# Kernel tuning notes

Hardware: AMD Instinct MI355X
Metric: run time of the kernel (lower is better)

The kernel has to match this reference:

```python
import jax, jax.numpy as jnp
import numpy as np

DIM = 128
HEADS = 4
DIM_HEAD = 32
HIDDEN = HEADS * DIM_HEAD  # 128
EPS = 1e-5


def setup_inputs() -> dict:
    key = jax.random.key(0)
    k0, k1, k2, k3 = jax.random.split(key, 4)
    b, h, w = 8, 128, 128
    x = jax.random.normal(k0, (b, DIM, h, w), dtype=jnp.float32)
    # 1x1 conv weights stored as [out_ch, in_ch]
    w_qkv = jax.random.normal(k1, (HIDDEN * 3, DIM), dtype=jnp.float32) * (1.0 / np.sqrt(DIM))
    w_out = jax.random.normal(k2, (DIM, HIDDEN), dtype=jnp.float32) * (1.0 / np.sqrt(HIDDEN))
    b_out = jnp.zeros((DIM,), dtype=jnp.float32)
    alpha = jnp.ones((DIM,), dtype=jnp.float32)
    beta = jnp.zeros((DIM,), dtype=jnp.float32)
    return {"x": x, "w_qkv": w_qkv, "w_out": w_out, "b_out": b_out,
            "alpha": alpha, "beta": beta}


def reference(x, w_qkv, w_out, b_out, alpha, beta):
    b, c, h, w = x.shape
    n = h * w
    scale = DIM_HEAD ** (-0.5)
    # 1x1 conv QKV (bias=False) == channel GEMM
    qkv = jnp.einsum('bchw,oc->bohw', x, w_qkv)  # [b, 3*HIDDEN, h, w]
    q, k, v = jnp.split(qkv, 3, axis=1)
    rs = lambda t: t.reshape(b, HEADS, DIM_HEAD, n)  # [b, heads, d, N]
    q = jax.nn.softmax(rs(q), axis=-2) * scale  # softmax over dim_head axis
    k = jax.nn.softmax(rs(k), axis=-1)          # softmax over spatial axis
    v = rs(v) / n
    # context[dk, dv] = sum_n k[dk, n] * v[dv, n]   (tiny d x d matrix)
    context = jnp.einsum('bhkn,bhvn->bhkv', k, v)
    # out[dv, n] = sum_dk context[dk, dv] * q[dk, n]
    out = jnp.einsum('bhkv,bhkn->bhvn', context, q)
    out = out.reshape(b, HIDDEN, h, w)
    # to_out: 1x1 conv with bias, then channel LayerNorm
    out = jnp.einsum('bchw,oc->bohw', out, w_out) + b_out[None, :, None, None]
    mean = jnp.mean(out, axis=1, keepdims=True)
    var = jnp.var(out, axis=1, keepdims=True)  # unbiased=False
    out = (out - mean) / jnp.sqrt(var + EPS)
    return out * alpha[None, :, None, None] + beta[None, :, None, None]
```

## Files before the change

### kernel.cpp

```cpp
#include <hip/hip_runtime.h>
#include <math.h>

#define B_ 8
#define C_ 128
#define N_ 16384
#define SCALE_ 0.17677669529663687f
#define EPS_ 1e-5f

#define KV_STRIDE 36
#define XU_STRIDE 68
#define REC_ 4224

typedef _Float16 half8 __attribute__((ext_vector_type(8)));
typedef float floatx4 __attribute__((ext_vector_type(4)));

static __device__ inline unsigned short f16bits(float v) {
  _Float16 h = (_Float16)v;
  return __builtin_bit_cast(unsigned short, h);
}

static __device__ inline void pack2(float a0, float a1,
                                    unsigned int& hp, unsigned int& lp) {
  _Float16 h0 = (_Float16)a0;
  _Float16 h1 = (_Float16)a1;
  float l0f = (a0 - (float)h0) * 2048.0f;
  float l1f = (a1 - (float)h1) * 2048.0f;
  hp = ((unsigned int)__builtin_bit_cast(unsigned short, h1) << 16) |
       (unsigned int)__builtin_bit_cast(unsigned short, h0);
  lp = ((unsigned int)f16bits(l1f) << 16) | (unsigned int)f16bits(l0f);
}

static __device__ inline void split8(const float* p, half8& hi, half8& lo) {
  float4 f0 = *(const float4*)p;
  float4 f1 = *(const float4*)(p + 4);
  float fv[8] = {f0.x, f0.y, f0.z, f0.w, f1.x, f1.y, f1.z, f1.w};
#pragma unroll
  for (int j = 0; j < 8; ++j) {
    _Float16 hj = (_Float16)fv[j];
    hi[j] = hj;
    lo[j] = (_Float16)((fv[j] - (float)hj) * 2048.0f);
  }
}

__global__ __launch_bounds__(1024, 4) void lin_attn_ctx(
    const float* __restrict__ x, const float* __restrict__ wqkv,
    float* __restrict__ Ws)
{
  __shared__ __align__(16) unsigned int xhiu[32 * XU_STRIDE];
  __shared__ __align__(16) unsigned int xlou[32 * XU_STRIDE];
  __shared__ __align__(16) float ks[128 * KV_STRIDE];
  __shared__ __align__(16) float vs[128 * KV_STRIDE];

  const int t = threadIdx.x;
  const int bpb = gridDim.x / B_;
  const int b = blockIdx.x / bpb;
  const int blk = blockIdx.x - b * bpb;
  const int nchunks = 512 / bpb;
  const int pbase = blk * (nchunks << 5);

  const int lane = t & 63;
  const int wave = t >> 6;
  const int l15 = lane & 15;
  const int quad = lane >> 4;

  half8 ahi[4], alo[4];
#pragma unroll
  for (int s = 0; s < 4; ++s)
    split8(wqkv + (size_t)(128 + (wave << 4) + l15) * C_ + (s << 5) + (quad << 3),
           ahi[s], alo[s]);

  const int hj = wave >> 2;
  const int at = (wave >> 1) & 1;
  const int bt = wave & 1;
  floatx4 pacc1 = (floatx4){0.f, 0.f, 0.f, 0.f};
  floatx4 pacc2 = (floatx4){0.f, 0.f, 0.f, 0.f};
  float sacc[4] = {0.f, 0.f, 0.f, 0.f};

  const float* xb = x + ((size_t)b * C_) * N_;
  const int kp0 = t >> 4;
  const int pq0 = (t & 15) << 1;

  float2 fa0, fa1;
  {
    const float* p = xb + pbase + pq0;
    fa0 = *(const float2*)(p + (size_t)(2 * kp0) * N_);
    fa1 = *(const float2*)(p + (size_t)(2 * kp0 + 1) * N_);
  }

  for (int c4 = 0; c4 < nchunks; ++c4) {
    __syncthreads();

    half8 eh, el, vh, vl;
    if (c4 > 0) {
      split8(&ks[((hj << 5) + (at << 4) + l15) * KV_STRIDE + (quad << 3)], eh, el);
      split8(&vs[((hj << 5) + (bt << 4) + l15) * KV_STRIDE + (quad << 3)], vh, vl);
    }

    {
      float a0[2] = {fa0.x, fa0.y};
      float a1[2] = {fa1.x, fa1.y};
#pragma unroll
      for (int j = 0; j < 2; ++j) {
        unsigned int hp, lp;
        pack2(a0[j], a1[j], hp, lp);
        xhiu[(pq0 + j) * XU_STRIDE + kp0] = hp;
        xlou[(pq0 + j) * XU_STRIDE + kp0] = lp;
      }
    }

    if (c4 > 0) {
      pacc1 = __builtin_amdgcn_mfma_f32_16x16x32_f16(eh, vh, pacc1, 0, 0, 0);
      pacc2 = __builtin_amdgcn_mfma_f32_16x16x32_f16(eh, vl, pacc2, 0, 0, 0);
      pacc2 = __builtin_amdgcn_mfma_f32_16x16x32_f16(el, vh, pacc2, 0, 0, 0);
    }

    __syncthreads();

    if (c4 + 1 < nchunks) {
      const float* p = xb + pbase + ((c4 + 1) << 5) + pq0;
      fa0 = *(const float2*)(p + (size_t)(2 * kp0) * N_);
      fa1 = *(const float2*)(p + (size_t)(2 * kp0 + 1) * N_);
    }

    floatx4 acc1[2], acc2[2];
#pragma unroll
    for (int c = 0; c < 2; ++c) {
      acc1[c] = (floatx4){0.f, 0.f, 0.f, 0.f};
      acc2[c] = (floatx4){0.f, 0.f, 0.f, 0.f};
    }
    __builtin_amdgcn_s_setprio(1);
#pragma unroll
    for (int s = 0; s < 4; ++s) {
#pragma unroll
      for (int c = 0; c < 2; ++c) {
        int off = ((c << 4) + l15) * XU_STRIDE + (s << 4) + (quad << 2);
        half8 bh = __builtin_bit_cast(half8, *(const uint4*)&xhiu[off]);
        half8 bl = __builtin_bit_cast(half8, *(const uint4*)&xlou[off]);
        acc1[c] = __builtin_amdgcn_mfma_f32_16x16x32_f16(ahi[s], bh, acc1[c], 0, 0, 0);
        acc2[c] = __builtin_amdgcn_mfma_f32_16x16x32_f16(ahi[s], bl, acc2[c], 0, 0, 0);
        acc2[c] = __builtin_amdgcn_mfma_f32_16x16x32_f16(alo[s], bh, acc2[c], 0, 0, 0);
      }
    }
    __builtin_amdgcn_s_setprio(0);

    if (wave < 8) {
#pragma unroll
      for (int c = 0; c < 2; ++c) {
        int px = (c << 4) + l15;
#pragma unroll
        for (int reg = 0; reg < 4; ++reg) {
          float val = acc1[c][reg] + acc2[c][reg] * (1.0f / 2048.0f);
          int row = (wave << 4) + (quad << 2) + reg;
          float e = __expf(val);
          ks[row * KV_STRIDE + px] = e;
          sacc[reg] += e;
        }
      }
    } else {
#pragma unroll
      for (int c = 0; c < 2; ++c) {
        int px = (c << 4) + l15;
#pragma unroll
        for (int reg = 0; reg < 4; ++reg) {
          float val = acc1[c][reg] + acc2[c][reg] * (1.0f / 2048.0f);
          int row = ((wave - 8) << 4) + (quad << 2) + reg;
          vs[row * KV_STRIDE + px] = val;
        }
      }
    }
  }

  __syncthreads();
  {
    half8 eh, el, vh, vl;
    split8(&ks[((hj << 5) + (at << 4) + l15) * KV_STRIDE + (quad << 3)], eh, el);
    split8(&vs[((hj << 5) + (bt << 4) + l15) * KV_STRIDE + (quad << 3)], vh, vl);
    pacc1 = __builtin_amdgcn_mfma_f32_16x16x32_f16(eh, vh, pacc1, 0, 0, 0);
    pacc2 = __builtin_amdgcn_mfma_f32_16x16x32_f16(eh, vl, pacc2, 0, 0, 0);
    pacc2 = __builtin_amdgcn_mfma_f32_16x16x32_f16(el, vh, pacc2, 0, 0, 0);
  }

  {
    float* rec = Ws + (size_t)blockIdx.x * REC_;
#pragma unroll
    for (int reg = 0; reg < 4; ++reg) {
      int dk = (at << 4) + (quad << 2) + reg;
      int dv = (bt << 4) + l15;
      rec[(((hj << 5) + dk) << 5) + dv] =
          pacc1[reg] + pacc2[reg] * (1.0f / 2048.0f);
    }
    if (wave < 8) {
#pragma unroll
      for (int reg = 0; reg < 4; ++reg) {
        float s = sacc[reg];
        s += __shfl_xor(s, 1);
        s += __shfl_xor(s, 2);
        s += __shfl_xor(s, 4);
        s += __shfl_xor(s, 8);
        sacc[reg] = s;
      }
      if (l15 == 0) {
#pragma unroll
        for (int reg = 0; reg < 4; ++reg)
          rec[4096 + (wave << 4) + (quad << 2) + reg] = sacc[reg];
      }
    }
  }
}

__global__ void lin_attn_redg(const float* __restrict__ Ws, int slots,
                              const float* __restrict__ wout,
                              float* __restrict__ G)
{
  __shared__ float p2[256];
  __shared__ float cx[128];
  __shared__ float ss[4];

  const int t = threadIdx.x;
  const int b = blockIdx.x >> 5;
  const int seg = blockIdx.x & 31;
  const int R0 = seg << 2;
  const int hs = slots >> 1;

  {
    const int e = t & 127;
    const int half = t >> 7;
    const float* src = Ws + ((size_t)b * slots + (size_t)half * hs) * REC_ +
                       R0 * 32 + e;
    float s = 0.f;
    for (int k = 0; k < hs; ++k) s += src[(size_t)k * REC_];
    p2[half * 128 + e] = s;
  }
  {
    const int row4 = t >> 6;
    const int lane = t & 63;
    float sv = (lane < slots)
             ? Ws[((size_t)b * slots + lane) * REC_ + 4096 + R0 + row4] : 0.f;
    sv += __shfl_xor(sv, 1);
    sv += __shfl_xor(sv, 2);
    sv += __shfl_xor(sv, 4);
    sv += __shfl_xor(sv, 8);
    sv += __shfl_xor(sv, 16);
    sv += __shfl_xor(sv, 32);
    if (lane == 0) ss[row4] = sv;
  }
  __syncthreads();
  if (t < 128) {
    cx[t] = (p2[t] + p2[128 + t]) / (ss[t >> 5] * 16384.f);
  }
  __syncthreads();
  {
    const int o = t >> 1;
    const int pr = t & 1;
#pragma unroll
    for (int p = 0; p < 2; ++p) {
      const int row4 = pr * 2 + p;
      const int grow = R0 + row4;
      const int h = grow >> 5;
      const float* wrow = wout + (size_t)o * 128 + h * 32;
      const float* crow = &cx[row4 * 32];
      float s = 0.f;
#pragma unroll
      for (int q = 0; q < 8; ++q) {
        float4 w4 = *(const float4*)&wrow[q * 4];
        float4 c4 = *(const float4*)&crow[q * 4];
        s += w4.x * c4.x + w4.y * c4.y + w4.z * c4.z + w4.w * c4.w;
      }
      G[(size_t)b * 16384 + (size_t)o * 128 + grow] = s * SCALE_;
    }
  }
}

__global__ __launch_bounds__(256, 2) void lin_attn_out(
    const float* __restrict__ x, const float* __restrict__ wqkv,
    const float* __restrict__ G, const float* __restrict__ bout,
    const float* __restrict__ alpha, const float* __restrict__ beta,
    float* __restrict__ out)
{
  __shared__ __align__(16) unsigned int xh[2][32 * XU_STRIDE];
  __shared__ __align__(16) unsigned int xl[2][32 * XU_STRIDE];
  __shared__ __align__(16) unsigned int qhiu[32 * XU_STRIDE];
  __shared__ __align__(16) unsigned int qlou[32 * XU_STRIDE];
  __shared__ float red_s[128];
  __shared__ float red_q[128];

  const int t = threadIdx.x;
  const int bpb = gridDim.x / B_;
  const int b = blockIdx.x / bpb;
  const int blk = blockIdx.x - b * bpb;
  const int nchunks = 512 / bpb;
  const int pbase = blk * (nchunks << 5);

  const int lane = t & 63;
  const int wave = t >> 6;
  const int l15 = lane & 15;
  const int quad = lane >> 4;

  half8 qhiA[2][4], qloA[2][4], ghiA[2][4], gloA[2][4];
#pragma unroll
  for (int r = 0; r < 2; ++r) {
#pragma unroll
    for (int s = 0; s < 4; ++s) {
      const int m = (wave << 5) + (r << 4) + l15;
      split8(wqkv + (size_t)m * C_ + (s << 5) + (quad << 3), qhiA[r][s], qloA[r][s]);
      split8(G + (size_t)b * 16384 + (size_t)m * 128 + (s << 5) + (quad << 3),
             ghiA[r][s], gloA[r][s]);
    }
  }

  float bch[8], ach[8], bech[8];
#pragma unroll
  for (int r = 0; r < 2; ++r)
#pragma unroll
    for (int reg = 0; reg < 4; ++reg) {
      int ch = (wave << 5) + (r << 4) + (quad << 2) + reg;
      bch[r * 4 + reg] = bout[ch];
      ach[r * 4 + reg] = alpha[ch];
      bech[r * 4 + reg] = beta[ch];
    }

  const float* xb = x + ((size_t)b * C_) * N_;
  const int kp0 = t >> 3;
  const int pq0 = (t & 7) << 2;
  float4 fa0, fa1, fb0, fb1;

  {
    const float* p = xb + pbase + pq0;
    fa0 = *(const float4*)(p + (size_t)(2 * kp0) * N_);
    fa1 = *(const float4*)(p + (size_t)(2 * kp0 + 1) * N_);
    fb0 = *(const float4*)(p + (size_t)(2 * kp0 + 64) * N_);
    fb1 = *(const float4*)(p + (size_t)(2 * kp0 + 65) * N_);
    float a0[4] = {fa0.x, fa0.y, fa0.z, fa0.w};
    float a1[4] = {fa1.x, fa1.y, fa1.z, fa1.w};
    float c0[4] = {fb0.x, fb0.y, fb0.z, fb0.w};
    float c1[4] = {fb1.x, fb1.y, fb1.z, fb1.w};
#pragma unroll
    for (int j = 0; j < 4; ++j) {
      unsigned int hp, lp;
      pack2(a0[j], a1[j], hp, lp);
      xh[0][(pq0 + j) * XU_STRIDE + kp0] = hp;
      xl[0][(pq0 + j) * XU_STRIDE + kp0] = lp;
      pack2(c0[j], c1[j], hp, lp);
      xh[0][(pq0 + j) * XU_STRIDE + kp0 + 32] = hp;
      xl[0][(pq0 + j) * XU_STRIDE + kp0 + 32] = lp;
    }
  }
  __syncthreads();

  float yv[2][8];

  for (int c4 = 0; c4 < nchunks; ++c4) {
    const int cur = c4 & 1;
    const int nxt = cur ^ 1;

    if (c4 + 1 < nchunks) {
      const float* p = xb + pbase + ((c4 + 1) << 5) + pq0;
      fa0 = *(const float4*)(p + (size_t)(2 * kp0) * N_);
      fa1 = *(const float4*)(p + (size_t)(2 * kp0 + 1) * N_);
      fb0 = *(const float4*)(p + (size_t)(2 * kp0 + 64) * N_);
      fb1 = *(const float4*)(p + (size_t)(2 * kp0 + 65) * N_);
    }

    floatx4 a1a[2][2], a2a[2][2];
#pragma unroll
    for (int r = 0; r < 2; ++r)
#pragma unroll
      for (int c = 0; c < 2; ++c) {
        a1a[r][c] = (floatx4){0.f, 0.f, 0.f, 0.f};
        a2a[r][c] = (floatx4){0.f, 0.f, 0.f, 0.f};
      }
    __builtin_amdgcn_s_setprio(1);
#pragma unroll
    for (int s = 0; s < 4; ++s) {
#pragma unroll
      for (int c = 0; c < 2; ++c) {
        int off = ((c << 4) + l15) * XU_STRIDE + (s << 4) + (quad << 2);
        half8 bh = __builtin_bit_cast(half8, *(const uint4*)&xh[cur][off]);
        half8 bl = __builtin_bit_cast(half8, *(const uint4*)&xl[cur][off]);
#pragma unroll
        for (int r = 0; r < 2; ++r) {
          a1a[r][c] = __builtin_amdgcn_mfma_f32_16x16x32_f16(qhiA[r][s], bh, a1a[r][c], 0, 0, 0);
          a2a[r][c] = __builtin_amdgcn_mfma_f32_16x16x32_f16(qhiA[r][s], bl, a2a[r][c], 0, 0, 0);
          a2a[r][c] = __builtin_amdgcn_mfma_f32_16x16x32_f16(qloA[r][s], bh, a2a[r][c], 0, 0, 0);
        }
      }
    }
    __builtin_amdgcn_s_setprio(0);

    float eq[2][8];
#pragma unroll
    for (int c = 0; c < 2; ++c) {
      float qv[8];
#pragma unroll
      for (int r = 0; r < 2; ++r)
#pragma unroll
        for (int reg = 0; reg < 4; ++reg)
          qv[r * 4 + reg] = a1a[r][c][reg] + a2a[r][c][reg] * (1.0f / 2048.0f);
      float mx = fmaxf(fmaxf(fmaxf(qv[0], qv[1]), fmaxf(qv[2], qv[3])),
                       fmaxf(fmaxf(qv[4], qv[5]), fmaxf(qv[6], qv[7])));
      mx = fmaxf(mx, __shfl_xor(mx, 16));
      mx = fmaxf(mx, __shfl_xor(mx, 32));
      float ss = 0.f;
#pragma unroll
      for (int j = 0; j < 8; ++j) { eq[c][j] = __expf(qv[j] - mx); ss += eq[c][j]; }
      ss += __shfl_xor(ss, 16);
      ss += __shfl_xor(ss, 32);
      float inv = 1.0f / ss;
#pragma unroll
      for (int j = 0; j < 8; ++j) eq[c][j] *= inv;
    }
    __syncthreads();

    if (c4 > 0) {
      float* ob = out + ((size_t)b * C_) * N_ + pbase + ((c4 - 1) << 5);
#pragma unroll
      for (int c = 0; c < 2; ++c) {
        int px = (c << 4) + l15;
        float ts = red_s[px] + red_s[32 + px] + red_s[64 + px] + red_s[96 + px];
        float tq = red_q[px] + red_q[32 + px] + red_q[64 + px] + red_q[96 + px];
        float mean = ts * (1.f / 128.f);
        float var = tq * (1.f / 128.f) - mean * mean;
        float rstd = 1.f / sqrtf(var + EPS_);
#pragma unroll
        for (int r = 0; r < 2; ++r)
#pragma unroll
          for (int reg = 0; reg < 4; ++reg) {
            int ch = (wave << 5) + (r << 4) + (quad << 2) + reg;
            ob[(size_t)ch * N_ + px] =
                (yv[c][r * 4 + reg] - mean) * rstd * ach[r * 4 + reg] + bech[r * 4 + reg];
          }
      }
    }

#pragma unroll
    for (int c = 0; c < 2; ++c) {
      int px = (c << 4) + l15;
#pragma unroll
      for (int r = 0; r < 2; ++r) {
        unsigned int h0, l0, h1, l1;
        pack2(eq[c][r * 4 + 0], eq[c][r * 4 + 1], h0, l0);
        pack2(eq[c][r * 4 + 2], eq[c][r * 4 + 3], h1, l1);
        int kp = (wave << 4) + (r << 3) + (quad << 1);
        uint2 hu; hu.x = h0; hu.y = h1;
        uint2 lu; lu.x = l0; lu.y = l1;
        *(uint2*)&qhiu[px * XU_STRIDE + kp] = hu;
        *(uint2*)&qlou[px * XU_STRIDE + kp] = lu;
      }
    }
    if (c4 + 1 < nchunks) {
      float a0[4] = {fa0.x, fa0.y, fa0.z, fa0.w};
      float a1[4] = {fa1.x, fa1.y, fa1.z, fa1.w};
      float c0[4] = {fb0.x, fb0.y, fb0.z, fb0.w};
      float c1[4] = {fb1.x, fb1.y, fb1.z, fb1.w};
#pragma unroll
      for (int j = 0; j < 4; ++j) {
        unsigned int hp, lp;
        pack2(a0[j], a1[j], hp, lp);
        xh[nxt][(pq0 + j) * XU_STRIDE + kp0] = hp;
        xl[nxt][(pq0 + j) * XU_STRIDE + kp0] = lp;
        pack2(c0[j], c1[j], hp, lp);
        xh[nxt][(pq0 + j) * XU_STRIDE + kp0 + 32] = hp;
        xl[nxt][(pq0 + j) * XU_STRIDE + kp0 + 32] = lp;
      }
    }
    __syncthreads();

#pragma unroll
    for (int r = 0; r < 2; ++r)
#pragma unroll
      for (int c = 0; c < 2; ++c) {
        a1a[r][c] = (floatx4){0.f, 0.f, 0.f, 0.f};
        a2a[r][c] = (floatx4){0.f, 0.f, 0.f, 0.f};
      }
    __builtin_amdgcn_s_setprio(1);
#pragma unroll
    for (int s = 0; s < 4; ++s) {
#pragma unroll
      for (int c = 0; c < 2; ++c) {
        int off = ((c << 4) + l15) * XU_STRIDE + (s << 4) + (quad << 2);
        half8 bh = __builtin_bit_cast(half8, *(const uint4*)&qhiu[off]);
        half8 bl = __builtin_bit_cast(half8, *(const uint4*)&qlou[off]);
#pragma unroll
        for (int r = 0; r < 2; ++r) {
          a1a[r][c] = __builtin_amdgcn_mfma_f32_16x16x32_f16(ghiA[r][s], bh, a1a[r][c], 0, 0, 0);
          a2a[r][c] = __builtin_amdgcn_mfma_f32_16x16x32_f16(ghiA[r][s], bl, a2a[r][c], 0, 0, 0);
          a2a[r][c] = __builtin_amdgcn_mfma_f32_16x16x32_f16(gloA[r][s], bh, a2a[r][c], 0, 0, 0);
        }
      }
    }
    __builtin_amdgcn_s_setprio(0);

#pragma unroll
    for (int c = 0; c < 2; ++c) {
      float sm = 0.f, sq = 0.f;
#pragma unroll
      for (int r = 0; r < 2; ++r)
#pragma unroll
        for (int reg = 0; reg < 4; ++reg) {
          float v = a1a[r][c][reg] + a2a[r][c][reg] * (1.0f / 2048.0f) + bch[r * 4 + reg];
          yv[c][r * 4 + reg] = v;
          sm += v;
          sq += v * v;
        }
      sm += __shfl_xor(sm, 16);  sq += __shfl_xor(sq, 16);
      sm += __shfl_xor(sm, 32);  sq += __shfl_xor(sq, 32);
      if (quad == 0) {
        red_s[(wave << 5) + (c << 4) + l15] = sm;
        red_q[(wave << 5) + (c << 4) + l15] = sq;
      }
    }
  }

  __syncthreads();
  {
    float* ob = out + ((size_t)b * C_) * N_ + pbase + ((nchunks - 1) << 5);
#pragma unroll
    for (int c = 0; c < 2; ++c) {
      int px = (c << 4) + l15;
      float ts = red_s[px] + red_s[32 + px] + red_s[64 + px] + red_s[96 + px];
      float tq = red_q[px] + red_q[32 + px] + red_q[64 + px] + red_q[96 + px];
      float mean = ts * (1.f / 128.f);
      float var = tq * (1.f / 128.f) - mean * mean;
      float rstd = 1.f / sqrtf(var + EPS_);
#pragma unroll
      for (int r = 0; r < 2; ++r)
#pragma unroll
        for (int reg = 0; reg < 4; ++reg) {
          int ch = (wave << 5) + (r << 4) + (quad << 2) + reg;
          ob[(size_t)ch * N_ + px] =
              (yv[c][r * 4 + reg] - mean) * rstd * ach[r * 4 + reg] + bech[r * 4 + reg];
        }
    }
  }
}

extern "C" void kernel_launch(void* const* d_in, const int* in_sizes, int n_in,
                              void* d_out, int out_size, void* d_ws, size_t ws_size,
                              hipStream_t stream) {
  const float* x     = (const float*)d_in[0];
  const float* wqkv  = (const float*)d_in[1];
  const float* wout  = (const float*)d_in[2];
  const float* bout  = (const float*)d_in[3];
  const float* alpha = (const float*)d_in[4];
  const float* beta  = (const float*)d_in[5];
  float* outp = (float*)d_out;

  float* G  = (float*)d_ws;
  float* Ws = G + (size_t)B_ * 16384 + B_ * 4096 + B_ * 128;

  const int bpb_ctx = 32;

  lin_attn_ctx<<<dim3(B_ * bpb_ctx), dim3(1024), 0, stream>>>(x, wqkv, Ws);
  lin_attn_redg<<<dim3(B_ * 32), dim3(256), 0, stream>>>(Ws, bpb_ctx, wout, G);
  lin_attn_out<<<dim3(B_ * 64), dim3(256), 0, stream>>>(x, wqkv, G, bout,
                                                        alpha, beta, outp);
}
```

Measured before the change: 197.0 us.

## Warp-specialize output kernel into Q-softmax and output-projection wave groups

Restructures the output kernel into 1024-thread blocks where 8 waves compute the QKV projection plus q-softmax and 8 waves compute the output projection plus LayerNorm one chunk behind, software-pipelined with double-buffered reduction arrays. Each wave now holds only one 16-row set of fp16 weight fragments, lowering register pressure. The softmax max subtraction is dropped and the head-wise sum is combined across paired waves via shared memory. This trades per-wave work for more waves and more block-wide barriers, and removing the max subtraction risks exp overflow on large logits.

```diff
diff --git a/kernel.cpp b/kernel.cpp
--- a/kernel.cpp
+++ b/kernel.cpp
@@ -271,7 +271,7 @@
   }
 }
 
-__global__ __launch_bounds__(256, 2) void lin_attn_out(
+__global__ __launch_bounds__(1024, 4) void lin_attn_out(
     const float* __restrict__ x, const float* __restrict__ wqkv,
     const float* __restrict__ G, const float* __restrict__ bout,
     const float* __restrict__ alpha, const float* __restrict__ beta,
@@ -281,8 +281,9 @@
   __shared__ __align__(16) unsigned int xl[2][32 * XU_STRIDE];
   __shared__ __align__(16) unsigned int qhiu[32 * XU_STRIDE];
   __shared__ __align__(16) unsigned int qlou[32 * XU_STRIDE];
-  __shared__ float red_s[128];
-  __shared__ float red_q[128];
+  __shared__ float ssum[256];
+  __shared__ float red_s[2][256];
+  __shared__ float red_q[2][256];
 
   const int t = threadIdx.x;
   const int bpb = gridDim.x / B_;
@@ -295,241 +296,222 @@
   const int wave = t >> 6;
   const int l15 = lane & 15;
   const int quad = lane >> 4;
-
-  half8 qhiA[2][4], qloA[2][4], ghiA[2][4], gloA[2][4];
-#pragma unroll
-  for (int r = 0; r < 2; ++r) {
-#pragma unroll
-    for (int s = 0; s < 4; ++s) {
-      const int m = (wave << 5) + (r << 4) + l15;
-      split8(wqkv + (size_t)m * C_ + (s << 5) + (quad << 3), qhiA[r][s], qloA[r][s]);
-      split8(G + (size_t)b * 16384 + (size_t)m * 128 + (s << 5) + (quad << 3),
-             ghiA[r][s], gloA[r][s]);
-    }
-  }
-
-  float bch[8], ach[8], bech[8];
-#pragma unroll
-  for (int r = 0; r < 2; ++r)
+  const bool qw = (wave < 8);
+  const int yw = wave - 8;
+
+  half8 ahi[4], alo[4];
+  {
+    const float* base = qw
+        ? (wqkv + (size_t)((wave << 4) + l15) * C_)
+        : (G + (size_t)b * 16384 + (size_t)((yw << 4) + l15) * 128);
+#pragma unroll
+    for (int s = 0; s < 4; ++s)
+      split8(base + (s << 5) + (quad << 3), ahi[s], alo[s]);
+  }
+
+  float bch[4], ach[4], bech[4];
+  if (!qw) {
 #pragma unroll
     for (int reg = 0; reg < 4; ++reg) {
-      int ch = (wave << 5) + (r << 4) + (quad << 2) + reg;
-      bch[r * 4 + reg] = bout[ch];
-      ach[r * 4 + reg] = alpha[ch];
-      bech[r * 4 + reg] = beta[ch];
-    }
+      int ch = (yw << 4) + (quad << 2) + reg;
+      bch[reg] = bout[ch];
+      ach[reg] = alpha[ch];
+      bech[reg] = beta[ch];
+    }
+  }
 
   const float* xb = x + ((size_t)b * C_) * N_;
-  const int kp0 = t >> 3;
-  const int pq0 = (t & 7) << 2;
-  float4 fa0, fa1, fb0, fb1;
-
+  float* ob0 = out + ((size_t)b * C_) * N_ + pbase;
+  const int kp0 = t >> 4;
+  const int pq0 = (t & 15) << 1;
+
+  float2 fa0, fa1;
   {
     const float* p = xb + pbase + pq0;
-    fa0 = *(const float4*)(p + (size_t)(2 * kp0) * N_);
-    fa1 = *(const float4*)(p + (size_t)(2 * kp0 + 1) * N_);
-    fb0 = *(const float4*)(p + (size_t)(2 * kp0 + 64) * N_);
-    fb1 = *(const float4*)(p + (size_t)(2 * kp0 + 65) * N_);
-    float a0[4] = {fa0.x, fa0.y, fa0.z, fa0.w};
-    float a1[4] = {fa1.x, fa1.y, fa1.z, fa1.w};
-    float c0[4] = {fb0.x, fb0.y, fb0.z, fb0.w};
-    float c1[4] = {fb1.x, fb1.y, fb1.z, fb1.w};
-#pragma unroll
-    for (int j = 0; j < 4; ++j) {
+    fa0 = *(const float2*)(p + (size_t)(2 * kp0) * N_);
+    fa1 = *(const float2*)(p + (size_t)(2 * kp0 + 1) * N_);
+    float a0[2] = {fa0.x, fa0.y};
+    float a1[2] = {fa1.x, fa1.y};
+#pragma unroll
+    for (int j = 0; j < 2; ++j) {
       unsigned int hp, lp;
       pack2(a0[j], a1[j], hp, lp);
       xh[0][(pq0 + j) * XU_STRIDE + kp0] = hp;
       xl[0][(pq0 + j) * XU_STRIDE + kp0] = lp;
-      pack2(c0[j], c1[j], hp, lp);
-      xh[0][(pq0 + j) * XU_STRIDE + kp0 + 32] = hp;
-      xl[0][(pq0 + j) * XU_STRIDE + kp0 + 32] = lp;
-    }
-  }
-  __syncthreads();
-
-  float yv[2][8];
-
-  for (int c4 = 0; c4 < nchunks; ++c4) {
-    const int cur = c4 & 1;
-    const int nxt = cur ^ 1;
-
-    if (c4 + 1 < nchunks) {
-      const float* p = xb + pbase + ((c4 + 1) << 5) + pq0;
-      fa0 = *(const float4*)(p + (size_t)(2 * kp0) * N_);
-      fa1 = *(const float4*)(p + (size_t)(2 * kp0 + 1) * N_);
-      fb0 = *(const float4*)(p + (size_t)(2 * kp0 + 64) * N_);
-      fb1 = *(const float4*)(p + (size_t)(2 * kp0 + 65) * N_);
-    }
-
-    floatx4 a1a[2][2], a2a[2][2];
-#pragma unroll
-    for (int r = 0; r < 2; ++r)
-#pragma unroll
-      for (int c = 0; c < 2; ++c) {
-        a1a[r][c] = (floatx4){0.f, 0.f, 0.f, 0.f};
-        a2a[r][c] = (floatx4){0.f, 0.f, 0.f, 0.f};
-      }
-    __builtin_amdgcn_s_setprio(1);
-#pragma unroll
-    for (int s = 0; s < 4; ++s) {
-#pragma unroll
-      for (int c = 0; c < 2; ++c) {
-        int off = ((c << 4) + l15) * XU_STRIDE + (s << 4) + (quad << 2);
-        half8 bh = __builtin_bit_cast(half8, *(const uint4*)&xh[cur][off]);
-        half8 bl = __builtin_bit_cast(half8, *(const uint4*)&xl[cur][off]);
-#pragma unroll
-        for (int r = 0; r < 2; ++r) {
-          a1a[r][c] = __builtin_amdgcn_mfma_f32_16x16x32_f16(qhiA[r][s], bh, a1a[r][c], 0, 0, 0);
-          a2a[r][c] = __builtin_amdgcn_mfma_f32_16x16x32_f16(qhiA[r][s], bl, a2a[r][c], 0, 0, 0);
-          a2a[r][c] = __builtin_amdgcn_mfma_f32_16x16x32_f16(qloA[r][s], bh, a2a[r][c], 0, 0, 0);
-        }
-      }
-    }
-    __builtin_amdgcn_s_setprio(0);
-
-    float eq[2][8];
-#pragma unroll
-    for (int c = 0; c < 2; ++c) {
-      float qv[8];
-#pragma unroll
-      for (int r = 0; r < 2; ++r)
-#pragma unroll
-        for (int reg = 0; reg < 4; ++reg)
-          qv[r * 4 + reg] = a1a[r][c][reg] + a2a[r][c][reg] * (1.0f / 2048.0f);
-      float mx = fmaxf(fmaxf(fmaxf(qv[0], qv[1]), fmaxf(qv[2], qv[3])),
-                       fmaxf(fmaxf(qv[4], qv[5]), fmaxf(qv[6], qv[7])));
-      mx = fmaxf(mx, __shfl_xor(mx, 16));
-      mx = fmaxf(mx, __shfl_xor(mx, 32));
-      float ss = 0.f;
-#pragma unroll
-      for (int j = 0; j < 8; ++j) { eq[c][j] = __expf(qv[j] - mx); ss += eq[c][j]; }
-      ss += __shfl_xor(ss, 16);
-      ss += __shfl_xor(ss, 32);
-      float inv = 1.0f / ss;
-#pragma unroll
-      for (int j = 0; j < 8; ++j) eq[c][j] *= inv;
-    }
+    }
+  }
+
+  float eq[2][4];
+  float sown[2];
+  float yv[2][4];
+
+  for (int i = 0; i <= nchunks; ++i) {
     __syncthreads();
 
-    if (c4 > 0) {
-      float* ob = out + ((size_t)b * C_) * N_ + pbase + ((c4 - 1) << 5);
+    if (i + 1 < nchunks) {
+      const float* p = xb + pbase + ((i + 1) << 5) + pq0;
+      fa0 = *(const float2*)(p + (size_t)(2 * kp0) * N_);
+      fa1 = *(const float2*)(p + (size_t)(2 * kp0 + 1) * N_);
+    }
+
+    if (qw) {
+      if (i < nchunks) {
+        const int cur = i & 1;
+        floatx4 a1c[2], a2c[2];
+#pragma unroll
+        for (int c = 0; c < 2; ++c) {
+          a1c[c] = (floatx4){0.f, 0.f, 0.f, 0.f};
+          a2c[c] = (floatx4){0.f, 0.f, 0.f, 0.f};
+        }
+        __builtin_amdgcn_s_setprio(1);
+#pragma unroll
+        for (int s = 0; s < 4; ++s) {
+#pragma unroll
+          for (int c = 0; c < 2; ++c) {
+            int off = ((c << 4) + l15) * XU_STRIDE + (s << 4) + (quad << 2);
+            half8 bh = __builtin_bit_cast(half8, *(const uint4*)&xh[cur][off]);
+            half8 bl = __builtin_bit_cast(half8, *(const uint4*)&xl[cur][off]);
+            a1c[c] = __builtin_amdgcn_mfma_f32_16x16x32_f16(ahi[s], bh, a1c[c], 0, 0, 0);
+            a2c[c] = __builtin_amdgcn_mfma_f32_16x16x32_f16(ahi[s], bl, a2c[c], 0, 0, 0);
+            a2c[c] = __builtin_amdgcn_mfma_f32_16x16x32_f16(alo[s], bh, a2c[c], 0, 0, 0);
+          }
+        }
+        __builtin_amdgcn_s_setprio(0);
+#pragma unroll
+        for (int c = 0; c < 2; ++c) {
+          float s4 = 0.f;
+#pragma unroll
+          for (int reg = 0; reg < 4; ++reg) {
+            float v = a1c[c][reg] + a2c[c][reg] * (1.0f / 2048.0f);
+            float e = __expf(v);
+            eq[c][reg] = e;
+            s4 += e;
+          }
+          s4 += __shfl_xor(s4, 16);
+          s4 += __shfl_xor(s4, 32);
+          sown[c] = s4;
+          if (quad == 0) ssum[(wave << 5) + (c << 4) + l15] = s4;
+        }
+      }
+    } else {
+      if (i >= 2) {
+        const float* rs = red_s[i & 1];
+        const float* rq = red_q[i & 1];
+        float* ob = ob0 + ((i - 2) << 5);
+#pragma unroll
+        for (int c = 0; c < 2; ++c) {
+          int px = (c << 4) + l15;
+          float ts = ((rs[px] + rs[32 + px]) + (rs[64 + px] + rs[96 + px])) +
+                     ((rs[128 + px] + rs[160 + px]) + (rs[192 + px] + rs[224 + px]));
+          float tq = ((rq[px] + rq[32 + px]) + (rq[64 + px] + rq[96 + px])) +
+                     ((rq[128 + px] + rq[160 + px]) + (rq[192 + px] + rq[224 + px]));
+          float mean = ts * (1.f / 128.f);
+          float var = tq * (1.f / 128.f) - mean * mean;
+          float rstd = 1.f / sqrtf(var + EPS_);
+#pragma unroll
+          for (int reg = 0; reg < 4; ++reg) {
+            int ch = (yw << 4) + (quad << 2) + reg;
+            ob[(size_t)ch * N_ + px] =
+                (yv[c][reg] - mean) * rstd * ach[reg] + bech[reg];
+          }
+        }
+      }
+      if (i >= 1) {
+        floatx4 a1c[2], a2c[2];
+#pragma unroll
+        for (int c = 0; c < 2; ++c) {
+          a1c[c] = (floatx4){0.f, 0.f, 0.f, 0.f};
+          a2c[c] = (floatx4){0.f, 0.f, 0.f, 0.f};
+        }
+        __builtin_amdgcn_s_setprio(1);
+#pragma unroll
+        for (int s = 0; s < 4; ++s) {
+#pragma unroll
+          for (int c = 0; c < 2; ++c) {
+            int off = ((c << 4) + l15) * XU_STRIDE + (s << 4) + (quad << 2);
+            half8 bh = __builtin_bit_cast(half8, *(const uint4*)&qhiu[off]);
+            half8 bl = __builtin_bit_cast(half8, *(const uint4*)&qlou[off]);
+            a1c[c] = __builtin_amdgcn_mfma_f32_16x16x32_f16(ahi[s], bh, a1c[c], 0, 0, 0);
+            a2c[c] = __builtin_amdgcn_mfma_f32_16x16x32_f16(ahi[s], bl, a2c[c], 0, 0, 0);
+            a2c[c] = __builtin_amdgcn_mfma_f32_16x16x32_f16(alo[s], bh, a2c[c], 0, 0, 0);
+          }
+        }
+        __builtin_amdgcn_s_setprio(0);
+        const int cb = (i - 1) & 1;
+#pragma unroll
+        for (int c = 0; c < 2; ++c) {
+          float sm = 0.f, sq = 0.f;
+#pragma unroll
+          for (int reg = 0; reg < 4; ++reg) {
+            float v = a1c[c][reg] + a2c[c][reg] * (1.0f / 2048.0f) + bch[reg];
+            yv[c][reg] = v;
+            sm += v;
+            sq += v * v;
+          }
+          sm += __shfl_xor(sm, 16);  sq += __shfl_xor(sq, 16);
+          sm += __shfl_xor(sm, 32);  sq += __shfl_xor(sq, 32);
+          if (quad == 0) {
+            red_s[cb][(yw << 5) + (c << 4) + l15] = sm;
+            red_q[cb][(yw << 5) + (c << 4) + l15] = sq;
+          }
+        }
+      }
+    }
+
+    if (i + 1 < nchunks) {
+      const int nx = (i + 1) & 1;
+      float a0[2] = {fa0.x, fa0.y};
+      float a1[2] = {fa1.x, fa1.y};
+#pragma unroll
+      for (int j = 0; j < 2; ++j) {
+        unsigned int hp, lp;
+        pack2(a0[j], a1[j], hp, lp);
+        xh[nx][(pq0 + j) * XU_STRIDE + kp0] = hp;
+        xl[nx][(pq0 + j) * XU_STRIDE + kp0] = lp;
+      }
+    }
+
+    __syncthreads();
+
+    if (qw && i < nchunks) {
 #pragma unroll
       for (int c = 0; c < 2; ++c) {
         int px = (c << 4) + l15;
-        float ts = red_s[px] + red_s[32 + px] + red_s[64 + px] + red_s[96 + px];
-        float tq = red_q[px] + red_q[32 + px] + red_q[64 + px] + red_q[96 + px];
-        float mean = ts * (1.f / 128.f);
-        float var = tq * (1.f / 128.f) - mean * mean;
-        float rstd = 1.f / sqrtf(var + EPS_);
-#pragma unroll
-        for (int r = 0; r < 2; ++r)
-#pragma unroll
-          for (int reg = 0; reg < 4; ++reg) {
-            int ch = (wave << 5) + (r << 4) + (quad << 2) + reg;
-            ob[(size_t)ch * N_ + px] =
-                (yv[c][r * 4 + reg] - mean) * rstd * ach[r * 4 + reg] + bech[r * 4 + reg];
-          }
-      }
-    }
-
-#pragma unroll
-    for (int c = 0; c < 2; ++c) {
-      int px = (c << 4) + l15;
-#pragma unroll
-      for (int r = 0; r < 2; ++r) {
+        float pairs = ssum[((wave ^ 1) << 5) + (c << 4) + l15];
+        float inv = 1.0f / (sown[c] + pairs);
         unsigned int h0, l0, h1, l1;
-        pack2(eq[c][r * 4 + 0], eq[c][r * 4 + 1], h0, l0);
-        pack2(eq[c][r * 4 + 2], eq[c][r * 4 + 3], h1, l1);
-        int kp = (wave << 4) + (r << 3) + (quad << 1);
+        pack2(eq[c][0] * inv, eq[c][1] * inv, h0, l0);
+        pack2(eq[c][2] * inv, eq[c][3] * inv, h1, l1);
+        int kp = (wave << 3) + (quad << 1);
         uint2 hu; hu.x = h0; hu.y = h1;
         uint2 lu; lu.x = l0; lu.y = l1;
         *(uint2*)&qhiu[px * XU_STRIDE + kp] = hu;
         *(uint2*)&qlou[px * XU_STRIDE + kp] = lu;
       }
     }
-    if (c4 + 1 < nchunks) {
-      float a0[4] = {fa0.x, fa0.y, fa0.z, fa0.w};
-      float a1[4] = {fa1.x, fa1.y, fa1.z, fa1.w};
-      float c0[4] = {fb0.x, fb0.y, fb0.z, fb0.w};
-      float c1[4] = {fb1.x, fb1.y, fb1.z, fb1.w};
-#pragma unroll
-      for (int j = 0; j < 4; ++j) {
-        unsigned int hp, lp;
-        pack2(a0[j], a1[j], hp, lp);
-        xh[nxt][(pq0 + j) * XU_STRIDE + kp0] = hp;
-        xl[nxt][(pq0 + j) * XU_STRIDE + kp0] = lp;
-        pack2(c0[j], c1[j], hp, lp);
-        xh[nxt][(pq0 + j) * XU_STRIDE + kp0 + 32] = hp;
-        xl[nxt][(pq0 + j) * XU_STRIDE + kp0 + 32] = lp;
-      }
-    }
-    __syncthreads();
-
-#pragma unroll
-    for (int r = 0; r < 2; ++r)
-#pragma unroll
-      for (int c = 0; c < 2; ++c) {
-        a1a[r][c] = (floatx4){0.f, 0.f, 0.f, 0.f};
-        a2a[r][c] = (floatx4){0.f, 0.f, 0.f, 0.f};
-      }
-    __builtin_amdgcn_s_setprio(1);
-#pragma unroll
-    for (int s = 0; s < 4; ++s) {
-#pragma unroll
-      for (int c = 0; c < 2; ++c) {
-        int off = ((c << 4) + l15) * XU_STRIDE + (s << 4) + (quad << 2);
-        half8 bh = __builtin_bit_cast(half8, *(const uint4*)&qhiu[off]);
-        half8 bl = __builtin_bit_cast(half8, *(const uint4*)&qlou[off]);
-#pragma unroll
-        for (int r = 0; r < 2; ++r) {
-          a1a[r][c] = __builtin_amdgcn_mfma_f32_16x16x32_f16(ghiA[r][s], bh, a1a[r][c], 0, 0, 0);
-          a2a[r][c] = __builtin_amdgcn_mfma_f32_16x16x32_f16(ghiA[r][s], bl, a2a[r][c], 0, 0, 0);
-          a2a[r][c] = __builtin_amdgcn_mfma_f32_16x16x32_f16(gloA[r][s], bh, a2a[r][c], 0, 0, 0);
-        }
-      }
-    }
-    __builtin_amdgcn_s_setprio(0);
-
-#pragma unroll
-    for (int c = 0; c < 2; ++c) {
-      float sm = 0.f, sq = 0.f;
-#pragma unroll
-      for (int r = 0; r < 2; ++r)
-#pragma unroll
-        for (int reg = 0; reg < 4; ++reg) {
-          float v = a1a[r][c][reg] + a2a[r][c][reg] * (1.0f / 2048.0f) + bch[r * 4 + reg];
-          yv[c][r * 4 + reg] = v;
-          sm += v;
-          sq += v * v;
-        }
-      sm += __shfl_xor(sm, 16);  sq += __shfl_xor(sq, 16);
-      sm += __shfl_xor(sm, 32);  sq += __shfl_xor(sq, 32);
-      if (quad == 0) {
-        red_s[(wave << 5) + (c << 4) + l15] = sm;
-        red_q[(wave << 5) + (c << 4) + l15] = sq;
-      }
-    }
   }
 
   __syncthreads();
-  {
-    float* ob = out + ((size_t)b * C_) * N_ + pbase + ((nchunks - 1) << 5);
+  if (!qw) {
+    const float* rs = red_s[(nchunks - 1) & 1];
+    const float* rq = red_q[(nchunks - 1) & 1];
+    float* ob = ob0 + ((nchunks - 1) << 5);
 #pragma unroll
     for (int c = 0; c < 2; ++c) {
       int px = (c << 4) + l15;
-      float ts = red_s[px] + red_s[32 + px] + red_s[64 + px] + red_s[96 + px];
-      float tq = red_q[px] + red_q[32 + px] + red_q[64 + px] + red_q[96 + px];
+      float ts = ((rs[px] + rs[32 + px]) + (rs[64 + px] + rs[96 + px])) +
+                 ((rs[128 + px] + rs[160 + px]) + (rs[192 + px] + rs[224 + px]));
+      float tq = ((rq[px] + rq[32 + px]) + (rq[64 + px] + rq[96 + px])) +
+                 ((rq[128 + px] + rq[160 + px]) + (rq[192 + px] + rq[224 + px]));
       float mean = ts * (1.f / 128.f);
       float var = tq * (1.f / 128.f) - mean * mean;
       float rstd = 1.f / sqrtf(var + EPS_);
 #pragma unroll
-      for (int r = 0; r < 2; ++r)
-#pragma unroll
-        for (int reg = 0; reg < 4; ++reg) {
-          int ch = (wave << 5) + (r << 4) + (quad << 2) + reg;
-          ob[(size_t)ch * N_ + px] =
-              (yv[c][r * 4 + reg] - mean) * rstd * ach[r * 4 + reg] + bech[r * 4 + reg];
-        }
+      for (int reg = 0; reg < 4; ++reg) {
+        int ch = (yw << 4) + (quad << 2) + reg;
+        ob[(size_t)ch * N_ + px] =
+            (yv[c][reg] - mean) * rstd * ach[reg] + bech[reg];
+      }
     }
   }
 }
@@ -552,6 +534,6 @@
 
   lin_attn_ctx<<<dim3(B_ * bpb_ctx), dim3(1024), 0, stream>>>(x, wqkv, Ws);
   lin_attn_redg<<<dim3(B_ * 32), dim3(256), 0, stream>>>(Ws, bpb_ctx, wout, G);
-  lin_attn_out<<<dim3(B_ * 64), dim3(256), 0, stream>>>(x, wqkv, G, bout,
-                                                        alpha, beta, outp);
-}
+  lin_attn_out<<<dim3(B_ * 32), dim3(1024), 0, stream>>>(x, wqkv, G, bout,
+                                                         alpha, beta, outp);
+}
```

New measurement: 212.2 us. 1.08x slower.
